# Optimization experiments

Measured on AMD Instinct MI355X. Metric: run time of the kernel, lower is better.

Reference implementation:

```python
import jax, jax.numpy as jnp
import numpy as np

COMMITMENT_COST = 0.25
EPS = 1e-10


def setup_inputs() -> dict:
    key = jax.random.key(0)
    k1, k2 = jax.random.split(key)
    inputs = jax.random.normal(k1, (8192, 8, 8, 8, 8), dtype=jnp.float32)
    codebook = jax.random.normal(k2, (512, 4096), dtype=jnp.float32)  # [E, D]
    return {"inputs": inputs, "codebook": codebook}


def reference(inputs, codebook):
    input_shape = inputs.shape
    B = input_shape[0]
    E, D = codebook.shape
    flat = inputs.reshape(B, -1)  # [B, D], D == embedding_dim

    distances = (
        jnp.sum(flat * flat, axis=1, keepdims=True)
        + jnp.sum(codebook * codebook, axis=1)
        - 2.0 * jnp.matmul(flat, codebook.T)
    )  # [B, E]

    encoding_indices = jnp.argmin(distances, axis=1)  # [B]
    encodings = jax.nn.one_hot(encoding_indices, E, dtype=inputs.dtype)  # [B, E]

    # Gather quantize (same math as encodings @ codebook)
    quantized = jnp.take(codebook, encoding_indices, axis=0).reshape(input_shape)

    e_latent_loss = jnp.mean((jax.lax.stop_gradient(quantized) - inputs) ** 2)
    q_latent_loss = jnp.mean((quantized - jax.lax.stop_gradient(inputs)) ** 2)
    loss = q_latent_loss + COMMITMENT_COST * e_latent_loss

    # Straight-through estimator
    quantized_st = inputs + jax.lax.stop_gradient(quantized - inputs)

    avg_probs = jnp.mean(encodings, axis=0)  # [E]
    perplexity = jnp.exp(-jnp.sum(avg_probs * jnp.log(avg_probs + EPS)))

    return (loss, quantized_st, perplexity, encodings)
```

## Files before the change

kernel.cpp:

```cpp
#include <hip/hip_runtime.h>
#include <stdint.h>

#define B_ROWS 8192
#define DIM 4096
#define E_CODES 512
#define MARGIN 16.0f

typedef __attribute__((ext_vector_type(8))) short short8;
typedef __attribute__((ext_vector_type(4))) float floatx4;

#define WS_SCORES 0
#define WS_ENORM  4194304
#define WS_COUNTS 4194816
#define WS_LOSS   4195328
#define WS_XNORM  4195329

#define O_LOSS 0
#define O_Q    1
#define O_PERP 33554433
#define O_ENC  33554434

__global__ __launch_bounds__(64) void k_enorm(const float* __restrict__ cb, float* __restrict__ enorm) {
    const int e = blockIdx.x;
    const int lane = threadIdx.x;
    const float4* c4 = (const float4*)(cb + (size_t)e * DIM);
    float p = 0.f;
#pragma unroll
    for (int j = 0; j < 16; j++) {
        float4 v = c4[j * 64 + lane];
        p = fmaf(v.x, v.x, fmaf(v.y, v.y, fmaf(v.z, v.z, fmaf(v.w, v.w, p))));
    }
    for (int off = 32; off; off >>= 1) p += __shfl_down(p, off);
    if (lane == 0) enorm[e] = p;
}

__device__ inline uint32_t pk2(float hi, float lo) {
    return __builtin_amdgcn_perm(__float_as_uint(hi), __float_as_uint(lo), 0x07060302u);
}

#define LDK 72
__global__ __launch_bounds__(512) void k_gemm(const float* __restrict__ X, const float* __restrict__ CB,
                                              float* __restrict__ scores, float* __restrict__ xnorm_sum) {
    __shared__ __align__(16) unsigned short As[64 * LDK];
    __shared__ __align__(16) unsigned short Bs[128 * LDK];
    __shared__ float xred[8];
    const int id = blockIdx.x;
    const int ks = id >> 9;
    const int h = id & 511;
    const int bn = (h >> 3) & 3;
    const int bm = ((h >> 5) << 3) | (h & 7);
    const int tid = threadIdx.x;
    const int lane = tid & 63;
    const int w = tid >> 6, wr = w >> 2, wc = w & 3;
    const int m16 = lane & 15, q4 = lane >> 4;

    const int rA = tid >> 3, cA = (tid & 7) * 8;
    const int rB = tid >> 2, cB = (tid & 3) * 16;
    const float* xg = X + (size_t)(bm * 64 + rA) * DIM + cA + (ks << 11);
    const float* cg = CB + (size_t)(bn * 128 + rB) * DIM + cB + (ks << 11);

    floatx4 acc[2][2];
#pragma unroll
    for (int i = 0; i < 2; i++)
#pragma unroll
        for (int j = 0; j < 2; j++) acc[i][j] = (floatx4){0.f, 0.f, 0.f, 0.f};
    float xn = 0.f;

    for (int kt = 0; kt < 2048; kt += 64) {
        const float4* xa = (const float4*)(xg + kt);
        const float4* ca = (const float4*)(cg + kt);
        float4 xv0 = xa[0], xv1 = xa[1];
        float4 cv0 = ca[0], cv1 = ca[1], cv2 = ca[2], cv3 = ca[3];
        xn = fmaf(xv0.x, xv0.x, fmaf(xv0.y, xv0.y, fmaf(xv0.z, xv0.z, fmaf(xv0.w, xv0.w, xn))));
        xn = fmaf(xv1.x, xv1.x, fmaf(xv1.y, xv1.y, fmaf(xv1.z, xv1.z, fmaf(xv1.w, xv1.w, xn))));
        __syncthreads();
        *(uint4*)(&As[rA * LDK + cA]) = make_uint4(pk2(xv0.y, xv0.x), pk2(xv0.w, xv0.z), pk2(xv1.y, xv1.x), pk2(xv1.w, xv1.z));
        *(uint4*)(&Bs[rB * LDK + cB])     = make_uint4(pk2(cv0.y, cv0.x), pk2(cv0.w, cv0.z), pk2(cv1.y, cv1.x), pk2(cv1.w, cv1.z));
        *(uint4*)(&Bs[rB * LDK + cB + 8]) = make_uint4(pk2(cv2.y, cv2.x), pk2(cv2.w, cv2.z), pk2(cv3.y, cv3.x), pk2(cv3.w, cv3.z));
        __syncthreads();
        short8 a[2][2], b[2][2];
#pragma unroll
        for (int i = 0; i < 2; i++)
#pragma unroll
            for (int kk = 0; kk < 2; kk++) {
                a[i][kk] = *(const short8*)(&As[(wr * 32 + i * 16 + m16) * LDK + kk * 32 + q4 * 8]);
                b[i][kk] = *(const short8*)(&Bs[(wc * 32 + i * 16 + m16) * LDK + kk * 32 + q4 * 8]);
            }
#pragma unroll
        for (int kk = 0; kk < 2; kk++)
#pragma unroll
            for (int i = 0; i < 2; i++)
#pragma unroll
                for (int j = 0; j < 2; j++)
                    acc[i][j] = __builtin_amdgcn_mfma_f32_16x16x32_bf16(a[i][kk], b[j][kk], acc[i][j], 0, 0, 0);
    }

#pragma unroll
    for (int j = 0; j < 2; j++) {
        const int col = bn * 128 + wc * 32 + j * 16 + m16;
#pragma unroll
        for (int i = 0; i < 2; i++) {
            const int row0 = bm * 64 + wr * 32 + i * 16 + q4 * 4;
#pragma unroll
            for (int rr = 0; rr < 4; rr++)
                atomicAdd(&scores[(size_t)(row0 + rr) * E_CODES + col], acc[i][j][rr]);
        }
    }

    for (int off = 32; off; off >>= 1) xn += __shfl_down(xn, off);
    if (lane == 0) xred[w] = xn;
    __syncthreads();
    if (tid == 0) {
        float s = 0.f;
        for (int k = 0; k < 8; k++) s += xred[k];
        atomicAdd(xnorm_sum, s);
    }
}

__global__ __launch_bounds__(256) void k_fused(const float* __restrict__ X, const float* __restrict__ CB,
                                               const float* __restrict__ scores, const float* __restrict__ enorm,
                                               int* __restrict__ counts, float* __restrict__ loss_sum,
                                               float* __restrict__ out) {
    const int tid = threadIdx.x;
    const int lane = tid & 63, w = tid >> 6;
    const int row = blockIdx.x * 4 + w;

    const float* sr = scores + (size_t)row * E_CODES;
    float s[8];
#pragma unroll
    for (int g = 0; g < 8; g++) s[g] = enorm[g * 64 + lane] - 2.0f * sr[g * 64 + lane];

    float mv = s[0]; int mi = lane;
#pragma unroll
    for (int g = 1; g < 8; g++) { if (s[g] < mv) { mv = s[g]; mi = g * 64 + lane; } }
    for (int off = 32; off; off >>= 1) {
        float ov = __shfl_xor(mv, off); int oi = __shfl_xor(mi, off);
        if (ov < mv || (ov == mv && oi < mi)) { mv = ov; mi = oi; }
    }
    const float thr = mv + MARGIN;

    unsigned long long bal[8]; int nc = 0;
#pragma unroll
    for (int g = 0; g < 8; g++) { bal[g] = __ballot(s[g] <= thr); nc += __popcll(bal[g]); }

    int beste = mi;
    if (nc > 1) {
        const float4* xr4 = (const float4*)(X + (size_t)row * DIM);
        float bestd = 3.0e38f; beste = 1 << 30;
#pragma unroll 1
        for (int g = 0; g < 8; g++) {
            unsigned long long mask = bal[g];
            while (mask) {
                const int b = __builtin_ctzll(mask); mask &= mask - 1;
                const int e = g * 64 + b;
                const float4* cr4 = (const float4*)(CB + (size_t)e * DIM);
                float p = 0.f;
#pragma unroll
                for (int i = 0; i < 16; i++) {
                    float4 x = xr4[i * 64 + lane];
                    float4 c = cr4[i * 64 + lane];
                    float dx = x.x - c.x, dy = x.y - c.y, dz = x.z - c.z, dw = x.w - c.w;
                    p = fmaf(dx, dx, fmaf(dy, dy, fmaf(dz, dz, fmaf(dw, dw, p))));
                }
                for (int off = 32; off; off >>= 1) p += __shfl_xor(p, off);
                if (p < bestd || (p == bestd && e < beste)) { bestd = p; beste = e; }
            }
        }
    }

    const float* cq = CB + (size_t)beste * DIM;
    float* oq = out + O_Q + (size_t)row * DIM;
#pragma unroll
    for (int i = 0; i < 64; i++) oq[i * 64 + lane] = cq[i * 64 + lane];

    float2* oe2 = (float2*)(out + O_ENC + (size_t)row * E_CODES);
#pragma unroll
    for (int k = 0; k < 4; k++) {
        const int e0 = (k * 64 + lane) * 2;
        float2 v; v.x = (e0 == beste) ? 1.0f : 0.0f; v.y = (e0 + 1 == beste) ? 1.0f : 0.0f;
        oe2[k * 64 + lane] = v;
    }

    if (lane == 0) {
        atomicAdd(&counts[beste], 1);
        const float ssel = enorm[beste] - 2.0f * sr[beste];
        atomicAdd(loss_sum, ssel);
    }
}

__global__ __launch_bounds__(512) void k_final(const int* __restrict__ counts, const float* __restrict__ loss_sum,
                                               const float* __restrict__ xnorm_sum, float* __restrict__ out) {
    const int tid = threadIdx.x;
    const int lane = tid & 63, w = tid >> 6;
    __shared__ float r[8];
    const float p = (float)counts[tid] * (1.0f / 8192.0f);
    float h = p * logf(p + 1e-10f);
    for (int off = 32; off; off >>= 1) h += __shfl_down(h, off);
    if (lane == 0) r[w] = h;
    __syncthreads();
    if (tid == 0) {
        float H = 0.f;
        for (int k = 0; k < 8; k++) H += r[k];
        out[O_PERP] = expf(-H);
        const float dist_total = loss_sum[0] + 0.25f * xnorm_sum[0];
        out[O_LOSS] = dist_total * (1.25f / 33554432.0f);
    }
}

extern "C" void kernel_launch(void* const* d_in, const int* in_sizes, int n_in,
                              void* d_out, int out_size, void* d_ws, size_t ws_size,
                              hipStream_t stream) {
    const float* X  = (const float*)d_in[0];
    const float* CB = (const float*)d_in[1];
    float* out = (float*)d_out;
    float* ws  = (float*)d_ws;
    float* scores = ws + WS_SCORES;
    float* enorm  = ws + WS_ENORM;
    int*   counts = (int*)(ws + WS_COUNTS);
    float* loss_s = ws + WS_LOSS;
    float* xnorm  = ws + WS_XNORM;

    hipMemsetAsync(scores, 0, (size_t)B_ROWS * E_CODES * sizeof(float), stream);
    hipMemsetAsync(counts, 0, (E_CODES + 2) * sizeof(int), stream);

    k_enorm<<<E_CODES, 64, 0, stream>>>(CB, enorm);
    k_gemm<<<1024, 512, 0, stream>>>(X, CB, scores, xnorm);
    k_fused<<<B_ROWS / 4, 256, 0, stream>>>(X, CB, scores, enorm, counts, loss_s, out);
    k_final<<<1, 512, 0, stream>>>(counts, loss_s, xnorm, out);
}
```

Before: 502.5 us.

## Pre-convert inputs to bf16 and use direct-to-LDS GEMM without split-K atomics

Adds conversion kernels that write bf16 copies of the inputs and codebook into unused output space, computing norms along the way. The GEMM then loads bf16 tiles straight into LDS with global_load_lds, uses a 128x64 tile over the full K, and writes enorm-adjusted distances directly instead of split-K atomic adds. This removes the scores memset, the atomics and the in-loop fp32-to-bf16 packing. The cost is an extra pass over the input to convert it, and the kernel relies on the output buffer as scratch before it is overwritten.

After: 468.4 us. -6.8%, faster.

```diff
diff --git a/kernel.cpp b/kernel.cpp
--- a/kernel.cpp
+++ b/kernel.cpp
@@ -19,106 +19,118 @@
 #define O_Q    1
 #define O_PERP 33554433
 #define O_ENC  33554434
-
-__global__ __launch_bounds__(64) void k_enorm(const float* __restrict__ cb, float* __restrict__ enorm) {
+#define XB_F_OFF  4
+#define CBB_F_OFF (4 + 16777216)
+
+__device__ inline uint32_t pk2(float hi, float lo) {
+    return __builtin_amdgcn_perm(__float_as_uint(hi), __float_as_uint(lo), 0x07060302u);
+}
+
+#define GLD_LDS16(g, l) \
+    __builtin_amdgcn_global_load_lds((const __attribute__((address_space(1))) void*)(g), \
+                                     (__attribute__((address_space(3))) void*)(l), 16, 0, 0)
+
+__global__ __launch_bounds__(256) void k_convert(const float* __restrict__ X,
+                                                 unsigned short* __restrict__ Xb,
+                                                 float* __restrict__ xnorm_sum) {
+    const int tid = threadIdx.x;
+    const int lane = tid & 63, w = tid >> 6;
+    const float4* x4 = (const float4*)X + (size_t)blockIdx.x * 4096;
+    uint2* o2 = (uint2*)Xb + (size_t)blockIdx.x * 4096;
+    float xn = 0.f;
+#pragma unroll
+    for (int i = 0; i < 16; i++) {
+        float4 v = x4[i * 256 + tid];
+        xn = fmaf(v.x, v.x, fmaf(v.y, v.y, fmaf(v.z, v.z, fmaf(v.w, v.w, xn))));
+        o2[i * 256 + tid] = make_uint2(pk2(v.y, v.x), pk2(v.w, v.z));
+    }
+    __shared__ float r[4];
+    for (int off = 32; off; off >>= 1) xn += __shfl_down(xn, off);
+    if (lane == 0) r[w] = xn;
+    __syncthreads();
+    if (tid == 0) atomicAdd(xnorm_sum, ((r[0] + r[1]) + r[2]) + r[3]);
+}
+
+__global__ __launch_bounds__(64) void k_cvt_cb(const float* __restrict__ CB,
+                                               unsigned short* __restrict__ CBb,
+                                               float* __restrict__ enorm) {
     const int e = blockIdx.x;
     const int lane = threadIdx.x;
-    const float4* c4 = (const float4*)(cb + (size_t)e * DIM);
+    const float4* c4 = (const float4*)CB + (size_t)e * 1024;
+    uint2* o2 = (uint2*)CBb + (size_t)e * 1024;
     float p = 0.f;
 #pragma unroll
-    for (int j = 0; j < 16; j++) {
-        float4 v = c4[j * 64 + lane];
+    for (int i = 0; i < 16; i++) {
+        float4 v = c4[i * 64 + lane];
         p = fmaf(v.x, v.x, fmaf(v.y, v.y, fmaf(v.z, v.z, fmaf(v.w, v.w, p))));
+        o2[i * 64 + lane] = make_uint2(pk2(v.y, v.x), pk2(v.w, v.z));
     }
     for (int off = 32; off; off >>= 1) p += __shfl_down(p, off);
     if (lane == 0) enorm[e] = p;
 }
 
-__device__ inline uint32_t pk2(float hi, float lo) {
-    return __builtin_amdgcn_perm(__float_as_uint(hi), __float_as_uint(lo), 0x07060302u);
-}
-
-#define LDK 72
-__global__ __launch_bounds__(512) void k_gemm(const float* __restrict__ X, const float* __restrict__ CB,
-                                              float* __restrict__ scores, float* __restrict__ xnorm_sum) {
-    __shared__ __align__(16) unsigned short As[64 * LDK];
-    __shared__ __align__(16) unsigned short Bs[128 * LDK];
-    __shared__ float xred[8];
-    const int id = blockIdx.x;
-    const int ks = id >> 9;
-    const int h = id & 511;
-    const int bn = (h >> 3) & 3;
-    const int bm = ((h >> 5) << 3) | (h & 7);
+__global__ __launch_bounds__(256) void k_gemm2(const unsigned short* __restrict__ Xb,
+                                               const unsigned short* __restrict__ CBb,
+                                               const float* __restrict__ enorm,
+                                               float* __restrict__ scores) {
+    __shared__ __align__(16) unsigned short As[128 * 32];
+    __shared__ __align__(16) unsigned short Bs[64 * 32];
+    const int h = blockIdx.x;
+    const int bn = (h >> 3) & 7;
+    const int bm = ((h >> 6) << 3) | (h & 7);
     const int tid = threadIdx.x;
     const int lane = tid & 63;
-    const int w = tid >> 6, wr = w >> 2, wc = w & 3;
+    const int w = tid >> 6, wr = w >> 1, wc = w & 1;
     const int m16 = lane & 15, q4 = lane >> 4;
 
-    const int rA = tid >> 3, cA = (tid & 7) * 8;
-    const int rB = tid >> 2, cB = (tid & 3) * 16;
-    const float* xg = X + (size_t)(bm * 64 + rA) * DIM + cA + (ks << 11);
-    const float* cg = CB + (size_t)(bn * 128 + rB) * DIM + cB + (ks << 11);
-
-    floatx4 acc[2][2];
-#pragma unroll
-    for (int i = 0; i < 2; i++)
-#pragma unroll
-        for (int j = 0; j < 2; j++) acc[i][j] = (floatx4){0.f, 0.f, 0.f, 0.f};
-    float xn = 0.f;
-
-    for (int kt = 0; kt < 2048; kt += 64) {
-        const float4* xa = (const float4*)(xg + kt);
-        const float4* ca = (const float4*)(cg + kt);
-        float4 xv0 = xa[0], xv1 = xa[1];
-        float4 cv0 = ca[0], cv1 = ca[1], cv2 = ca[2], cv3 = ca[3];
-        xn = fmaf(xv0.x, xv0.x, fmaf(xv0.y, xv0.y, fmaf(xv0.z, xv0.z, fmaf(xv0.w, xv0.w, xn))));
-        xn = fmaf(xv1.x, xv1.x, fmaf(xv1.y, xv1.y, fmaf(xv1.z, xv1.z, fmaf(xv1.w, xv1.w, xn))));
+    const int lr = lane >> 2, lc = (lane & 3) * 8;
+    const unsigned short* xg0 = Xb + (size_t)(bm * 128 + w * 32 + lr) * DIM + lc;
+    const unsigned short* xg1 = xg0 + 16 * DIM;
+    const unsigned short* bg  = CBb + (size_t)(bn * 64 + w * 16 + lr) * DIM + lc;
+    unsigned short* lA0 = &As[(2 * w) * 512];
+    unsigned short* lA1 = &As[(2 * w + 1) * 512];
+    unsigned short* lB  = &Bs[w * 512];
+
+    floatx4 acc[4][2];
+#pragma unroll
+    for (int f = 0; f < 4; f++)
+#pragma unroll
+        for (int j = 0; j < 2; j++) acc[f][j] = (floatx4){0.f, 0.f, 0.f, 0.f};
+
+    for (int kt = 0; kt < DIM; kt += 32) {
+        GLD_LDS16(xg0 + kt, lA0);
+        GLD_LDS16(xg1 + kt, lA1);
+        GLD_LDS16(bg + kt, lB);
         __syncthreads();
-        *(uint4*)(&As[rA * LDK + cA]) = make_uint4(pk2(xv0.y, xv0.x), pk2(xv0.w, xv0.z), pk2(xv1.y, xv1.x), pk2(xv1.w, xv1.z));
-        *(uint4*)(&Bs[rB * LDK + cB])     = make_uint4(pk2(cv0.y, cv0.x), pk2(cv0.w, cv0.z), pk2(cv1.y, cv1.x), pk2(cv1.w, cv1.z));
-        *(uint4*)(&Bs[rB * LDK + cB + 8]) = make_uint4(pk2(cv2.y, cv2.x), pk2(cv2.w, cv2.z), pk2(cv3.y, cv3.x), pk2(cv3.w, cv3.z));
+        short8 a[4], b[2];
+#pragma unroll
+        for (int f = 0; f < 4; f++) a[f] = *(const short8*)(&As[(wr * 64 + f * 16 + m16) * 32 + q4 * 8]);
+#pragma unroll
+        for (int j = 0; j < 2; j++) b[j] = *(const short8*)(&Bs[(wc * 32 + j * 16 + m16) * 32 + q4 * 8]);
+#pragma unroll
+        for (int f = 0; f < 4; f++)
+#pragma unroll
+            for (int j = 0; j < 2; j++)
+                acc[f][j] = __builtin_amdgcn_mfma_f32_16x16x32_bf16(a[f], b[j], acc[f][j], 0, 0, 0);
         __syncthreads();
-        short8 a[2][2], b[2][2];
-#pragma unroll
-        for (int i = 0; i < 2; i++)
-#pragma unroll
-            for (int kk = 0; kk < 2; kk++) {
-                a[i][kk] = *(const short8*)(&As[(wr * 32 + i * 16 + m16) * LDK + kk * 32 + q4 * 8]);
-                b[i][kk] = *(const short8*)(&Bs[(wc * 32 + i * 16 + m16) * LDK + kk * 32 + q4 * 8]);
-            }
-#pragma unroll
-        for (int kk = 0; kk < 2; kk++)
-#pragma unroll
-            for (int i = 0; i < 2; i++)
-#pragma unroll
-                for (int j = 0; j < 2; j++)
-                    acc[i][j] = __builtin_amdgcn_mfma_f32_16x16x32_bf16(a[i][kk], b[j][kk], acc[i][j], 0, 0, 0);
     }
 
 #pragma unroll
     for (int j = 0; j < 2; j++) {
-        const int col = bn * 128 + wc * 32 + j * 16 + m16;
-#pragma unroll
-        for (int i = 0; i < 2; i++) {
-            const int row0 = bm * 64 + wr * 32 + i * 16 + q4 * 4;
+        const int col = bn * 64 + wc * 32 + j * 16 + m16;
+        const float en = enorm[col];
+#pragma unroll
+        for (int f = 0; f < 4; f++) {
+            const int row0 = bm * 128 + wr * 64 + f * 16 + q4 * 4;
 #pragma unroll
             for (int rr = 0; rr < 4; rr++)
-                atomicAdd(&scores[(size_t)(row0 + rr) * E_CODES + col], acc[i][j][rr]);
+                scores[(size_t)(row0 + rr) * E_CODES + col] = en - 2.0f * acc[f][j][rr];
         }
     }
-
-    for (int off = 32; off; off >>= 1) xn += __shfl_down(xn, off);
-    if (lane == 0) xred[w] = xn;
-    __syncthreads();
-    if (tid == 0) {
-        float s = 0.f;
-        for (int k = 0; k < 8; k++) s += xred[k];
-        atomicAdd(xnorm_sum, s);
-    }
 }
 
 __global__ __launch_bounds__(256) void k_fused(const float* __restrict__ X, const float* __restrict__ CB,
-                                               const float* __restrict__ scores, const float* __restrict__ enorm,
+                                               const float* __restrict__ scores,
                                                int* __restrict__ counts, float* __restrict__ loss_sum,
                                                float* __restrict__ out) {
     const int tid = threadIdx.x;
@@ -128,7 +140,7 @@
     const float* sr = scores + (size_t)row * E_CODES;
     float s[8];
 #pragma unroll
-    for (int g = 0; g < 8; g++) s[g] = enorm[g * 64 + lane] - 2.0f * sr[g * 64 + lane];
+    for (int g = 0; g < 8; g++) s[g] = sr[g * 64 + lane];
 
     float mv = s[0]; int mi = lane;
 #pragma unroll
@@ -183,8 +195,7 @@
 
     if (lane == 0) {
         atomicAdd(&counts[beste], 1);
-        const float ssel = enorm[beste] - 2.0f * sr[beste];
-        atomicAdd(loss_sum, ssel);
+        atomicAdd(loss_sum, sr[beste]);
     }
 }
 
@@ -202,7 +213,7 @@
         float H = 0.f;
         for (int k = 0; k < 8; k++) H += r[k];
         out[O_PERP] = expf(-H);
-        const float dist_total = loss_sum[0] + 0.25f * xnorm_sum[0];
+        const float dist_total = loss_sum[0] + xnorm_sum[0];
         out[O_LOSS] = dist_total * (1.25f / 33554432.0f);
     }
 }
@@ -219,12 +230,14 @@
     int*   counts = (int*)(ws + WS_COUNTS);
     float* loss_s = ws + WS_LOSS;
     float* xnorm  = ws + WS_XNORM;
-
-    hipMemsetAsync(scores, 0, (size_t)B_ROWS * E_CODES * sizeof(float), stream);
+    unsigned short* Xb  = (unsigned short*)(out + XB_F_OFF);
+    unsigned short* CBb = (unsigned short*)(out + CBB_F_OFF);
+
     hipMemsetAsync(counts, 0, (E_CODES + 2) * sizeof(int), stream);
 
-    k_enorm<<<E_CODES, 64, 0, stream>>>(CB, enorm);
-    k_gemm<<<1024, 512, 0, stream>>>(X, CB, scores, xnorm);
-    k_fused<<<B_ROWS / 4, 256, 0, stream>>>(X, CB, scores, enorm, counts, loss_s, out);
+    k_convert<<<2048, 256, 0, stream>>>(X, Xb, xnorm);
+    k_cvt_cb<<<E_CODES, 64, 0, stream>>>(CB, CBb, enorm);
+    k_gemm2<<<512, 256, 0, stream>>>(Xb, CBb, enorm, scores);
+    k_fused<<<B_ROWS / 4, 256, 0, stream>>>(X, CB, scores, counts, loss_s, out);
     k_final<<<1, 512, 0, stream>>>(counts, loss_s, xnorm, out);
 }
```
